# Performance work log

Hardware: AMD Instinct MI355X
Metric: run time of the kernel (lower is better)

Reference implementation:

```python
import jax, jax.numpy as jnp
import numpy as np

N = 20000   # nodes
E = 200000  # edges
D = 32      # inp_dim == out_dim == emb_dim
R = 100     # num_rel
EPS = 1e-5  # BatchNorm1d default eps


def setup_inputs() -> dict:
    key = jax.random.key(0)
    ks = jax.random.split(key, 5)
    h = jax.random.normal(ks[0], (N, D), dtype=jnp.float32)
    # xavier_uniform-ish scale for [R, D, D] relation weights
    weight = jax.random.normal(ks[1], (R, D, D), dtype=jnp.float32) * (1.0 / np.sqrt(D))
    gamma = jnp.ones((D,), dtype=jnp.float32)
    beta = jnp.zeros((D,), dtype=jnp.float32)
    src = jax.random.randint(ks[2], (E,), 0, N, dtype=jnp.int32)
    dst = jax.random.randint(ks[3], (E,), 0, N, dtype=jnp.int32)
    etype = jax.random.randint(ks[4], (E,), 0, R, dtype=jnp.int32)
    return {"h": h, "weight": weight, "gamma": gamma, "beta": beta,
            "src": src, "dst": dst, "etype": etype}


def reference(h, weight, gamma, beta, src, dst, etype):
    # per-edge relation-weight gather: [E, D, D]
    w_e = weight[etype]
    # per-edge bmm (src feature row-vector @ relation matrix) + relu: [E, D]
    msg = jax.nn.relu(jnp.einsum('ed,edo->eo', h[src], w_e))
    # BatchNorm1d in training mode: batch stats over the edge dimension
    mu = jnp.mean(msg, axis=0)
    var = jnp.mean(jnp.square(msg - mu), axis=0)  # biased variance
    msg = (msg - mu) * jax.lax.rsqrt(var + EPS) * gamma + beta
    # segment-mean reduce of messages into destination nodes: [N, D]
    ssum = jax.ops.segment_sum(msg, dst, num_segments=N)
    cnt = jax.ops.segment_sum(jnp.ones((E,), msg.dtype), dst, num_segments=N)
    return ssum / jnp.maximum(cnt, 1.0)[:, None]
```

## Files before the change

kernel.cpp:

```cpp
#include <hip/hip_runtime.h>

#define D 32
#define EPS 1e-5f
#define TPB 256
#define NB 256

__global__ void hist2_kernel(const int* __restrict__ etype, int E, int R, int chunk,
                             int* __restrict__ blockHistT)
{
    __shared__ int lh[1024];
    for (int i = threadIdx.x; i < R; i += TPB) lh[i] = 0;
    __syncthreads();
    const int lo = blockIdx.x * chunk, hi = min(E, lo + chunk);
    for (int e = lo + threadIdx.x; e < hi; e += TPB)
        atomicAdd(&lh[etype[e]], 1);
    __syncthreads();
    for (int r = threadIdx.x; r < R; r += TPB)
        blockHistT[r * NB + blockIdx.x] = lh[r];
}

__global__ void scan2_kernel(int* __restrict__ blockHistT, int R,
                             int* __restrict__ rel_start,
                             int* __restrict__ task_rel, int* __restrict__ task_start,
                             int* __restrict__ n_tasks)
{
    __shared__ int tot[1024];
    __shared__ int s_start[1025];
    __shared__ int s_tbase[1024];
    const int r = threadIdx.x;
    if (r < R) {
        int acc = 0;
        int* p = blockHistT + r * NB;
        for (int b = 0; b < NB; ++b) { int v = p[b]; p[b] = acc; acc += v; }
        tot[r] = acc;
    }
    __syncthreads();
    if (threadIdx.x == 0) {
        int acc = 0, tb = 0;
        for (int rr = 0; rr < R; ++rr) {
            s_start[rr] = acc; s_tbase[rr] = tb;
            acc += tot[rr];
            tb  += (tot[rr] + TPB - 1) / TPB;
        }
        s_start[R] = acc;
        rel_start[R] = acc;
        *n_tasks = tb;
    }
    __syncthreads();
    if (r < R) {
        const int st = s_start[r];
        rel_start[r] = st;
        const int nb = (tot[r] + TPB - 1) / TPB;
        const int tb = s_tbase[r];
        for (int b = 0; b < nb; ++b) {
            task_rel[tb + b]   = r;
            task_start[tb + b] = st + b * TPB;
        }
    }
}

__global__ void scatter2_kernel(const int* __restrict__ src, const int* __restrict__ dst,
                                const int* __restrict__ etype, int E, int R, int chunk,
                                const int* __restrict__ blockHistT,
                                const int* __restrict__ rel_start,
                                int* __restrict__ ssrc, int* __restrict__ sdst)
{
    __shared__ int cur[1024];
    for (int r = threadIdx.x; r < R; r += TPB)
        cur[r] = rel_start[r] + blockHistT[r * NB + blockIdx.x];
    __syncthreads();
    const int lo = blockIdx.x * chunk, hi = min(E, lo + chunk);
    for (int e = lo + threadIdx.x; e < hi; e += TPB) {
        const int p = atomicAdd(&cur[etype[e]], 1);
        ssrc[p] = src[e];
        sdst[p] = dst[e];
    }
}

__global__ __launch_bounds__(TPB)
void rgcn_main(const float* __restrict__ h, const float* __restrict__ W,
               const int* __restrict__ rel_start,
               const int* __restrict__ task_rel, const int* __restrict__ task_start,
               const int* __restrict__ n_tasks_p,
               const int* __restrict__ ssrc, const int* __restrict__ sdst,
               float* __restrict__ out,
               float* __restrict__ stat_sum, float* __restrict__ stat_sq,
               float* __restrict__ cnt)
{
    __shared__ float s_tile[TPB * 33];
    __shared__ int   s_src[TPB];
    __shared__ int   s_dst[TPB];
    __shared__ float s_aux[2 * TPB];

    const int task = blockIdx.x;
    if (task >= *n_tasks_p) return;
    const int r      = task_rel[task];
    const int start  = task_start[task];
    const int relEnd = rel_start[r + 1];
    const int nE     = min(TPB, relEnd - start);
    const int tid    = threadIdx.x;

    if (tid < nE) {
        s_src[tid] = ssrc[start + tid];
        s_dst[tid] = sdst[start + tid];
    }
    __syncthreads();

    for (int i = tid; i < nE * 8; i += TPB) {
        const int row = i >> 3, seg = i & 7;
        const float4 v = *(const float4*)(h + (size_t)s_src[row] * D + seg * 4);
        float* p = &s_tile[row * 33 + seg * 4];
        p[0] = v.x; p[1] = v.y; p[2] = v.z; p[3] = v.w;
    }
    __syncthreads();

    const float* Wr = W + (size_t)__builtin_amdgcn_readfirstlane(r) * (D * D);

    float acc[D];
#pragma unroll
    for (int o = 0; o < D; ++o) acc[o] = 0.f;

    if (tid < nE) {
#pragma unroll 4
        for (int d = 0; d < D; ++d) {
            const float hd = s_tile[tid * 33 + d];
#pragma unroll
            for (int o = 0; o < D; ++o)
                acc[o] = fmaf(hd, Wr[d * D + o], acc[o]);
        }
#pragma unroll
        for (int o = 0; o < D; ++o) acc[o] = fmaxf(acc[o], 0.f);
        atomicAdd(&cnt[s_dst[tid]], 1.0f);
    }
    __syncthreads();

    if (tid < nE) {
#pragma unroll
        for (int o = 0; o < D; ++o) s_tile[tid * 33 + o] = acc[o];
    }
    __syncthreads();

    float ps = 0.f, pq = 0.f;
    for (int i = tid; i < nE * D; i += TPB) {
        const int row = i >> 5, o = i & 31;
        const float v = s_tile[row * 33 + o];
        atomicAdd(&out[(size_t)s_dst[row] * D + o], v);
        ps += v; pq += v * v;
    }
    s_aux[tid]       = ps;
    s_aux[TPB + tid] = pq;
    __syncthreads();
    if (tid < D) {
        float ss = 0.f, sq = 0.f;
#pragma unroll
        for (int c = 0; c < TPB / D; ++c) {
            ss += s_aux[c * D + tid];
            sq += s_aux[TPB + c * D + tid];
        }
        atomicAdd(&stat_sum[tid], ss);
        atomicAdd(&stat_sq[tid], sq);
    }
}

__global__ void finalize_kernel(float* __restrict__ out, const float* __restrict__ cnt,
                                const float* __restrict__ stat_sum,
                                const float* __restrict__ stat_sq,
                                const float* __restrict__ gamma,
                                const float* __restrict__ beta,
                                float invE, int total)
{
    const int i = blockIdx.x * TPB + threadIdx.x;
    if (i >= total) return;
    const int o    = i & 31;
    const int node = i >> 5;
    const float mu  = stat_sum[o] * invE;
    const float var = fmaxf(stat_sq[o] * invE - mu * mu, 0.f);
    const float is  = rsqrtf(var + EPS);
    const float sc  = gamma[o] * is;
    const float sh  = fmaf(-mu, sc, beta[o]);
    const float c   = cnt[node];
    out[i] = fmaf(out[i], sc, sh * c) / fmaxf(c, 1.0f);
}

extern "C" void kernel_launch(void* const* d_in, const int* in_sizes, int n_in,
                              void* d_out, int out_size, void* d_ws, size_t ws_size,
                              hipStream_t stream)
{
    const float* h     = (const float*)d_in[0];
    const float* W     = (const float*)d_in[1];
    const float* gamma = (const float*)d_in[2];
    const float* beta  = (const float*)d_in[3];
    const int*   src   = (const int*)d_in[4];
    const int*   dst   = (const int*)d_in[5];
    const int*   etype = (const int*)d_in[6];
    float* out = (float*)d_out;

    const int E = in_sizes[4];
    const int N = in_sizes[0] / D;
    const int R = in_sizes[1] / (D * D);
    const int T = R + (E + TPB - 1) / TPB;
    const int chunk = (E + NB - 1) / NB;

    float* stat_sum  = (float*)d_ws;
    float* stat_sq   = stat_sum + D;
    float* cnt       = stat_sq + D;
    int*   rel_start = (int*)(cnt + N);
    int*   n_tasks   = rel_start + R + 1;
    int*   task_rel  = n_tasks + 1;
    int*   task_start= task_rel + T;
    int*   blockHistT= task_start + T;
    int*   ssrc      = blockHistT + R * NB;
    int*   sdst      = ssrc + E;

    hipMemsetAsync(d_ws, 0, sizeof(float) * (size_t)(2 * D + N), stream);
    hipMemsetAsync(d_out, 0, sizeof(float) * (size_t)out_size, stream);

    hist2_kernel<<<NB, TPB, 0, stream>>>(etype, E, R, chunk, blockHistT);
    scan2_kernel<<<1, TPB, 0, stream>>>(blockHistT, R, rel_start,
                                        task_rel, task_start, n_tasks);
    scatter2_kernel<<<NB, TPB, 0, stream>>>(src, dst, etype, E, R, chunk,
                                            blockHistT, rel_start, ssrc, sdst);
    rgcn_main<<<T, TPB, 0, stream>>>(h, W, rel_start, task_rel, task_start,
                                     n_tasks, ssrc, sdst, out,
                                     stat_sum, stat_sq, cnt);
    finalize_kernel<<<(N * D + TPB - 1) / TPB, TPB, 0, stream>>>(
        out, cnt, stat_sum, stat_sq, gamma, beta, 1.0f / (float)E, N * D);
}
```

Measured before the change: 153.1 us.

## Replace atomic scatter with dst-sorted CSR gather reduction and parallel relation scan

Instead of atomically adding each message into the output, the compute kernel writes per-edge messages to a buffer. A counting sort by destination (node counts, a single-block scan, and an atomic scatter into a permutation) then builds CSR offsets, and a gather kernel sums each node's messages and applies the batch-norm and mean in one pass. The per-relation prefix scan is split into a parallel per-relation block scan plus a small serial pass. This removes global float atomics on the output and the separate finalize and output memset. In exchange it adds a 25.6 MB message buffer round-trip, several extra launches, and a serial single-block node scan over 20k entries.

```diff
diff --git a/kernel.cpp b/kernel.cpp
--- a/kernel.cpp
+++ b/kernel.cpp
@@ -5,7 +5,7 @@
 #define TPB 256
 #define NB 256
 
-__global__ void hist2_kernel(const int* __restrict__ etype, int E, int R, int chunk,
+__global__ void histE_kernel(const int* __restrict__ etype, int E, int R, int chunk,
                              int* __restrict__ blockHistT)
 {
     __shared__ int lh[1024];
@@ -19,38 +19,51 @@
         blockHistT[r * NB + blockIdx.x] = lh[r];
 }
 
-__global__ void scan2_kernel(int* __restrict__ blockHistT, int R,
-                             int* __restrict__ rel_start,
-                             int* __restrict__ task_rel, int* __restrict__ task_start,
-                             int* __restrict__ n_tasks)
-{
-    __shared__ int tot[1024];
-    __shared__ int s_start[1025];
+__global__ void scanEa_kernel(int* __restrict__ blockHistT, int* __restrict__ relTot)
+{
+    __shared__ int buf[NB];
+    int* p = blockHistT + blockIdx.x * NB;
+    const int t = threadIdx.x;
+    const int v = p[t];
+    buf[t] = v;
+    __syncthreads();
+    int x = v;
+    for (int off = 1; off < NB; off <<= 1) {
+        const int y = (t >= off) ? buf[t - off] : 0;
+        __syncthreads();
+        x += y;
+        buf[t] = x;
+        __syncthreads();
+    }
+    p[t] = x - v;
+    if (t == NB - 1) relTot[blockIdx.x] = x;
+}
+
+__global__ void scanEb_kernel(const int* __restrict__ relTot, int R,
+                              int* __restrict__ rel_start,
+                              int* __restrict__ task_rel, int* __restrict__ task_start,
+                              int* __restrict__ n_tasks)
+{
+    __shared__ int s_tot[1024];
+    __shared__ int s_start[1024];
     __shared__ int s_tbase[1024];
-    const int r = threadIdx.x;
-    if (r < R) {
-        int acc = 0;
-        int* p = blockHistT + r * NB;
-        for (int b = 0; b < NB; ++b) { int v = p[b]; p[b] = acc; acc += v; }
-        tot[r] = acc;
-    }
+    for (int r = threadIdx.x; r < R; r += TPB) s_tot[r] = relTot[r];
     __syncthreads();
     if (threadIdx.x == 0) {
         int acc = 0, tb = 0;
-        for (int rr = 0; rr < R; ++rr) {
-            s_start[rr] = acc; s_tbase[rr] = tb;
-            acc += tot[rr];
-            tb  += (tot[rr] + TPB - 1) / TPB;
-        }
-        s_start[R] = acc;
+        for (int r = 0; r < R; ++r) {
+            s_start[r] = acc; s_tbase[r] = tb;
+            acc += s_tot[r];
+            tb  += (s_tot[r] + TPB - 1) / TPB;
+        }
         rel_start[R] = acc;
         *n_tasks = tb;
     }
     __syncthreads();
-    if (r < R) {
+    for (int r = threadIdx.x; r < R; r += TPB) {
         const int st = s_start[r];
         rel_start[r] = st;
-        const int nb = (tot[r] + TPB - 1) / TPB;
+        const int nb = (s_tot[r] + TPB - 1) / TPB;
         const int tb = s_tbase[r];
         for (int b = 0; b < nb; ++b) {
             task_rel[tb + b]   = r;
@@ -59,11 +72,12 @@
     }
 }
 
-__global__ void scatter2_kernel(const int* __restrict__ src, const int* __restrict__ dst,
+__global__ void scatterE_kernel(const int* __restrict__ src, const int* __restrict__ dst,
                                 const int* __restrict__ etype, int E, int R, int chunk,
                                 const int* __restrict__ blockHistT,
                                 const int* __restrict__ rel_start,
-                                int* __restrict__ ssrc, int* __restrict__ sdst)
+                                int* __restrict__ ssrc, int* __restrict__ sdst,
+                                int* __restrict__ nodeCnt)
 {
     __shared__ int cur[1024];
     for (int r = threadIdx.x; r < R; r += TPB)
@@ -71,25 +85,59 @@
     __syncthreads();
     const int lo = blockIdx.x * chunk, hi = min(E, lo + chunk);
     for (int e = lo + threadIdx.x; e < hi; e += TPB) {
+        const int d = dst[e];
         const int p = atomicAdd(&cur[etype[e]], 1);
         ssrc[p] = src[e];
-        sdst[p] = dst[e];
+        sdst[p] = d;
+        atomicAdd(&nodeCnt[d], 1);
+    }
+}
+
+__global__ void scanD_kernel(const int* __restrict__ nodeCnt, int N, int E,
+                             int* __restrict__ node_start, int* __restrict__ curD)
+{
+    __shared__ int part[TPB];
+    __shared__ int base[TPB];
+    const int per = (N + TPB - 1) / TPB;
+    const int lo = threadIdx.x * per, hi = min(N, lo + per);
+    int s = 0;
+    for (int n = lo; n < hi; ++n) s += nodeCnt[n];
+    part[threadIdx.x] = s;
+    __syncthreads();
+    if (threadIdx.x == 0) {
+        int a = 0;
+        for (int t = 0; t < TPB; ++t) { base[t] = part[t]; part[t] = a; a += base[t]; }
+    }
+    __syncthreads();
+    int a = part[threadIdx.x];
+    for (int n = lo; n < hi; ++n) {
+        node_start[n] = a;
+        curD[n] = a;
+        a += nodeCnt[n];
+    }
+    if (threadIdx.x == TPB - 1) node_start[N] = E;
+}
+
+__global__ void scatterD_kernel(const int* __restrict__ sdst, int E,
+                                int* __restrict__ curD, int* __restrict__ perm)
+{
+    for (int j = blockIdx.x * TPB + threadIdx.x; j < E; j += gridDim.x * TPB) {
+        const int p = atomicAdd(&curD[sdst[j]], 1);
+        perm[p] = j;
     }
 }
 
 __global__ __launch_bounds__(TPB)
-void rgcn_main(const float* __restrict__ h, const float* __restrict__ W,
-               const int* __restrict__ rel_start,
-               const int* __restrict__ task_rel, const int* __restrict__ task_start,
-               const int* __restrict__ n_tasks_p,
-               const int* __restrict__ ssrc, const int* __restrict__ sdst,
-               float* __restrict__ out,
-               float* __restrict__ stat_sum, float* __restrict__ stat_sq,
-               float* __restrict__ cnt)
+void rgcn_compute(const float* __restrict__ h, const float* __restrict__ W,
+                  const int* __restrict__ rel_start,
+                  const int* __restrict__ task_rel, const int* __restrict__ task_start,
+                  const int* __restrict__ n_tasks_p,
+                  const int* __restrict__ ssrc,
+                  float* __restrict__ msg,
+                  float* __restrict__ stat_sum, float* __restrict__ stat_sq)
 {
     __shared__ float s_tile[TPB * 33];
     __shared__ int   s_src[TPB];
-    __shared__ int   s_dst[TPB];
     __shared__ float s_aux[2 * TPB];
 
     const int task = blockIdx.x;
@@ -100,10 +148,7 @@
     const int nE     = min(TPB, relEnd - start);
     const int tid    = threadIdx.x;
 
-    if (tid < nE) {
-        s_src[tid] = ssrc[start + tid];
-        s_dst[tid] = sdst[start + tid];
-    }
+    if (tid < nE) s_src[tid] = ssrc[start + tid];
     __syncthreads();
 
     for (int i = tid; i < nE * 8; i += TPB) {
@@ -130,7 +175,6 @@
         }
 #pragma unroll
         for (int o = 0; o < D; ++o) acc[o] = fmaxf(acc[o], 0.f);
-        atomicAdd(&cnt[s_dst[tid]], 1.0f);
     }
     __syncthreads();
 
@@ -141,10 +185,11 @@
     __syncthreads();
 
     float ps = 0.f, pq = 0.f;
+    float* mbase = msg + (size_t)start * D;
     for (int i = tid; i < nE * D; i += TPB) {
         const int row = i >> 5, o = i & 31;
         const float v = s_tile[row * 33 + o];
-        atomicAdd(&out[(size_t)s_dst[row] * D + o], v);
+        mbase[i] = v;
         ps += v; pq += v * v;
     }
     s_aux[tid]       = ps;
@@ -158,28 +203,34 @@
             sq += s_aux[TPB + c * D + tid];
         }
         atomicAdd(&stat_sum[tid], ss);
-        atomicAdd(&stat_sq[tid], sq);
-    }
-}
-
-__global__ void finalize_kernel(float* __restrict__ out, const float* __restrict__ cnt,
-                                const float* __restrict__ stat_sum,
-                                const float* __restrict__ stat_sq,
-                                const float* __restrict__ gamma,
-                                const float* __restrict__ beta,
-                                float invE, int total)
-{
-    const int i = blockIdx.x * TPB + threadIdx.x;
-    if (i >= total) return;
-    const int o    = i & 31;
-    const int node = i >> 5;
+        atomicAdd(&stat_sq[tid],  sq);
+    }
+}
+
+__global__ void reduce_kernel(const float* __restrict__ msg, const int* __restrict__ perm,
+                              const int* __restrict__ node_start,
+                              const float* __restrict__ stat_sum,
+                              const float* __restrict__ stat_sq,
+                              const float* __restrict__ gamma,
+                              const float* __restrict__ beta,
+                              float invE, float* __restrict__ out, int N)
+{
+    const int o = threadIdx.x & 31;
+    const int n = blockIdx.x * 8 + (threadIdx.x >> 5);
+    if (n >= N) return;
+    const int j0 = node_start[n], j1 = node_start[n + 1];
+    float s = 0.f;
+    for (int j = j0; j < j1; ++j) {
+        const int e = perm[j];
+        s += msg[(size_t)e * D + o];
+    }
     const float mu  = stat_sum[o] * invE;
     const float var = fmaxf(stat_sq[o] * invE - mu * mu, 0.f);
     const float is  = rsqrtf(var + EPS);
     const float sc  = gamma[o] * is;
     const float sh  = fmaf(-mu, sc, beta[o]);
-    const float c   = cnt[node];
-    out[i] = fmaf(out[i], sc, sh * c) / fmaxf(c, 1.0f);
+    const float c   = (float)(j1 - j0);
+    out[(size_t)n * D + o] = fmaf(s, sc, sh * c) / fmaxf(c, 1.0f);
 }
 
 extern "C" void kernel_launch(void* const* d_in, const int* in_sizes, int n_in,
@@ -201,28 +252,35 @@
     const int T = R + (E + TPB - 1) / TPB;
     const int chunk = (E + NB - 1) / NB;
 
-    float* stat_sum  = (float*)d_ws;
+    int*   nodeCnt   = (int*)d_ws;
+    float* stat_sum  = (float*)(nodeCnt + N);
     float* stat_sq   = stat_sum + D;
-    float* cnt       = stat_sq + D;
-    int*   rel_start = (int*)(cnt + N);
+    int*   node_start= (int*)(stat_sq + D);
+    int*   curD      = node_start + N + 1;
+    int*   relTot    = curD + N;
+    int*   rel_start = relTot + R;
     int*   n_tasks   = rel_start + R + 1;
-    int*   task_rel  = n_tasks + 1;
+    int*   blockHistT= n_tasks + 1;
+    int*   task_rel  = blockHistT + R * NB;
     int*   task_start= task_rel + T;
-    int*   blockHistT= task_start + T;
-    int*   ssrc      = blockHistT + R * NB;
+    int*   ssrc      = task_start + T;
     int*   sdst      = ssrc + E;
-
-    hipMemsetAsync(d_ws, 0, sizeof(float) * (size_t)(2 * D + N), stream);
-    hipMemsetAsync(d_out, 0, sizeof(float) * (size_t)out_size, stream);
-
-    hist2_kernel<<<NB, TPB, 0, stream>>>(etype, E, R, chunk, blockHistT);
-    scan2_kernel<<<1, TPB, 0, stream>>>(blockHistT, R, rel_start,
-                                        task_rel, task_start, n_tasks);
-    scatter2_kernel<<<NB, TPB, 0, stream>>>(src, dst, etype, E, R, chunk,
-                                            blockHistT, rel_start, ssrc, sdst);
-    rgcn_main<<<T, TPB, 0, stream>>>(h, W, rel_start, task_rel, task_start,
-                                     n_tasks, ssrc, sdst, out,
-                                     stat_sum, stat_sq, cnt);
-    finalize_kernel<<<(N * D + TPB - 1) / TPB, TPB, 0, stream>>>(
-        out, cnt, stat_sum, stat_sq, gamma, beta, 1.0f / (float)E, N * D);
-}
+    int*   perm      = sdst + E;
+    float* msg       = (float*)(perm + E);
+
+    hipMemsetAsync(d_ws, 0, sizeof(int) * (size_t)(N + 2 * D), stream);
+
+    histE_kernel<<<NB, TPB, 0, stream>>>(etype, E, R, chunk, blockHistT);
+    scanEa_kernel<<<R, TPB, 0, stream>>>(blockHistT, relTot);
+    scanEb_kernel<<<1, TPB, 0, stream>>>(relTot, R, rel_start,
+                                         task_rel, task_start, n_tasks);
+    scatterE_kernel<<<NB, TPB, 0, stream>>>(src, dst, etype, E, R, chunk,
+                                            blockHistT, rel_start, ssrc, sdst, nodeCnt);
+    scanD_kernel<<<1, TPB, 0, stream>>>(nodeCnt, N, E, node_start, curD);
+    rgcn_compute<<<T, TPB, 0, stream>>>(h, W, rel_start, task_rel, task_start,
+                                        n_tasks, ssrc, msg, stat_sum, stat_sq);
+    scatterD_kernel<<<NB, TPB, 0, stream>>>(sdst, E, curD, perm);
+    reduce_kernel<<<(N + 7) / 8, TPB, 0, stream>>>(msg, perm, node_start,
+                                                   stat_sum, stat_sq, gamma, beta,
+                                                   1.0f / (float)E, out, N);
+}
```

After: 196.6 us. 1.28x slower.
